# Kernel optimization log

Hardware: AMD Instinct MI355X
Metric: run time of the kernel (lower is better)

Reference implementation:

```python
import jax, jax.numpy as jnp
import numpy as np

B, T, D, L, H = 4096, 200, 128, 64, 128  # n_traj, time steps, input_dim, latent_dim, n_units


def _lin(key, fan_in, fan_out):
    s = 1.0 / np.sqrt(fan_in)
    kw, kb = jax.random.split(key)
    w = jax.random.uniform(kw, (fan_in, fan_out), jnp.float32, -s, s)
    b = jax.random.uniform(kb, (fan_out,), jnp.float32, -s, s)
    return w, b


def setup_inputs() -> dict:
    key = jax.random.key(0)
    ks = jax.random.split(key, 8)
    data = jax.random.normal(ks[0], (B, T, D), jnp.float32)
    time_steps = jax.random.uniform(ks[1], (T,), jnp.float32)
    cin = 2 * L + D
    ug_w1, ug_b1 = _lin(ks[2], cin, H)
    ug_w2, ug_b2 = _lin(ks[3], H, L)
    rg_w1, rg_b1 = _lin(ks[4], cin, H)
    rg_w2, rg_b2 = _lin(ks[5], H, L)
    ns_w1, ns_b1 = _lin(ks[6], cin, H)
    ns_w2, ns_b2 = _lin(ks[7], H, 2 * L)
    return dict(data=data, time_steps=time_steps,
                ug_w1=ug_w1, ug_b1=ug_b1, ug_w2=ug_w2, ug_b2=ug_b2,
                rg_w1=rg_w1, rg_b1=rg_b1, rg_w2=rg_w2, rg_b2=rg_b2,
                ns_w1=ns_w1, ns_b1=ns_b1, ns_w2=ns_w2, ns_b2=ns_b2)


def reference(data, time_steps,
              ug_w1, ug_b1, ug_w2, ug_b2,
              rg_w1, rg_b1, rg_w2, rg_b2,
              ns_w1, ns_b1, ns_w2, ns_b2):
    # GRUUnit (latent-ODE style): gates are 2-layer MLPs (Tanh hidden) over
    # concat([y_mean, y_logvar, x]); update/reset end in Sigmoid, new_state
    # net emits 2L (mean, |std|).
    def step(carry, x):  # x: [B, D]
        y, s = carry  # each [B, L]
        h = jnp.concatenate([y, s, x], axis=-1)  # [B, 2L+D]
        u = jax.nn.sigmoid(jnp.tanh(h @ ug_w1 + ug_b1) @ ug_w2 + ug_b2)
        r = jax.nn.sigmoid(jnp.tanh(h @ rg_w1 + rg_b1) @ rg_w2 + rg_b2)
        hc = jnp.concatenate([y * r, s * r, x], axis=-1)
        ns = jnp.tanh(hc @ ns_w1 + ns_b1) @ ns_w2 + ns_b2  # [B, 2L]
        new_mean = ns[:, :L]
        new_std = jnp.abs(ns[:, L:])
        y2 = (1.0 - u) * new_mean + u * y
        s2 = (1.0 - u) * new_std + u * s
        return (y2, s2), None

    y0 = jnp.zeros((data.shape[0], L), data.dtype)
    s0 = jnp.zeros((data.shape[0], L), data.dtype)
    xs = jnp.transpose(data, (1, 0, 2))  # [T, B, D]; scan over time
    (yT, sT), _ = jax.lax.scan(step, (y0, s0), xs)
    return yT, sT
```

## Files before the change

### kernel.cpp

```cpp
#include <hip/hip_runtime.h>
#include <hip/hip_bf16.h>


#define NB 4096
#define NT 200
#define ND 128
#define HS 528
#define TS 272

typedef __bf16 bf16;
typedef __attribute__((ext_vector_type(8))) __bf16 bf16x8;
typedef __attribute__((ext_vector_type(4))) __bf16 bf16x4;
typedef __attribute__((ext_vector_type(4))) float f32x4;

#define BAR() asm volatile("s_waitcnt lgkmcnt(0)\n\ts_barrier" ::: "memory")

__device__ __forceinline__ f32x4 mfma16(bf16x8 a, bf16x8 b, f32x4 c){
    return __builtin_amdgcn_mfma_f32_16x16x32_bf16(a, b, c, 0, 0, 0);
}
__device__ __forceinline__ float fast_tanh(float x){
    float e = __expf(2.f * x);
    return 1.f - 2.f * __builtin_amdgcn_rcpf(e + 1.f);
}
__device__ __forceinline__ float fast_sigmoid(float x){
    return __builtin_amdgcn_rcpf(1.f + __expf(-x));
}
__device__ __forceinline__ bf16x4 tanh4(f32x4 a){
    bf16x4 o;
    o[0] = (bf16)fast_tanh(a[0]);
    o[1] = (bf16)fast_tanh(a[1]);
    o[2] = (bf16)fast_tanh(a[2]);
    o[3] = (bf16)fast_tanh(a[3]);
    return o;
}
__device__ __forceinline__ f32x4 bias4(const float* b, int f){
    f32x4 r; r[0]=b[f]; r[1]=b[f+1]; r[2]=b[f+2]; r[3]=b[f+3]; return r;
}

__global__ __launch_bounds__(512, 2)
void vae_rnn(const float* __restrict__ data,
             const float* __restrict__ ug_w1, const float* __restrict__ ug_b1,
             const float* __restrict__ ug_w2, const float* __restrict__ ug_b2,
             const float* __restrict__ rg_w1, const float* __restrict__ rg_b1,
             const float* __restrict__ rg_w2, const float* __restrict__ rg_b2,
             const float* __restrict__ ns_w1, const float* __restrict__ ns_b1,
             const float* __restrict__ ns_w2, const float* __restrict__ ns_b2,
             float* __restrict__ out)
{
    __shared__ __align__(16) char h_lds [16 * HS];
    __shared__ __align__(16) char t_lds [16 * HS];
    __shared__ __align__(16) char tn_lds[16 * TS];
    __shared__ float u_lds[16][68];

    const int tid  = threadIdx.x;
    const int w    = tid >> 6;
    const int lane = tid & 63;
    const int lq   = lane >> 4;
    const int lc   = lane & 15;
    const int row0 = blockIdx.x * 16;

    const bool UG = (w < 4);
    const int fA = w * 32;
    const int fB = (w & 3) * 16;
    const int fC = w * 16;
    const int fD = w * 16;

    const float* W1 = UG ? ug_w1 : rg_w1;
    const float* B1 = UG ? ug_b1 : rg_b1;
    const float* W2 = UG ? ug_w2 : rg_w2;
    const float* B2 = UG ? ug_b2 : rg_b2;

    bf16x8 wAy[8], wAx[8]; f32x4 bA[2];
    #pragma unroll
    for (int j = 0; j < 2; ++j){
        int n = (fA + j*16 + lc) & 127;
        bA[j] = bias4(B1, (fA + j*16 + lq*4) & 127);
        #pragma unroll
        for (int kt = 0; kt < 4; ++kt){
            bf16x8 fy, fx;
            #pragma unroll
            for (int e = 0; e < 8; ++e){
                fy[e] = (bf16)W1[(      kt*32 + lq*8 + e)*128 + n];
                fx[e] = (bf16)W1[(128 + kt*32 + lq*8 + e)*128 + n];
            }
            wAy[kt*2 + j] = fy; wAx[kt*2 + j] = fx;
        }
    }
    bf16x8 wB[4]; f32x4 bB = bias4(B2, fB + lq*4);
    {
        int n = fB + lc;
        #pragma unroll
        for (int kt = 0; kt < 4; ++kt){
            bf16x8 f;
            #pragma unroll
            for (int e = 0; e < 8; ++e) f[e] = (bf16)W2[(kt*32 + lq*8 + e)*64 + n];
            wB[kt] = f;
        }
    }
    bf16x8 wCh[4], wCx[4]; f32x4 bC = bias4(ns_b1, fC + lq*4);
    {
        int n = fC + lc;
        #pragma unroll
        for (int kt = 0; kt < 4; ++kt){
            bf16x8 fh, fx;
            #pragma unroll
            for (int e = 0; e < 8; ++e){
                fh[e] = (bf16)ns_w1[(      kt*32 + lq*8 + e)*128 + n];
                fx[e] = (bf16)ns_w1[(128 + kt*32 + lq*8 + e)*128 + n];
            }
            wCh[kt] = fh; wCx[kt] = fx;
        }
    }
    bf16x8 wD[4]; f32x4 bD = bias4(ns_b2, fD + lq*4);
    {
        int n = fD + lc;
        #pragma unroll
        for (int kt = 0; kt < 4; ++kt){
            bf16x8 f;
            #pragma unroll
            for (int e = 0; e < 8; ++e) f[e] = (bf16)ns_w2[(kt*32 + lq*8 + e)*128 + n];
            wD[kt] = f;
        }
    }

    const char* h_ys_rd = h_lds + lc*HS + lq*16;
    const char* h_x_rd  = h_lds + lc*HS + 256 + lq*16;
    char*       t_wr    = t_lds + lc*HS + 2*(fA + lq*4);
    const char* t_rd    = t_lds + lc*HS + lq*16 + (UG ? 0 : 256);
    char*       tn_wr   = tn_lds + lc*TS + 2*(fC + lq*4);
    const char* tn_rd   = tn_lds + lc*TS + lq*16;
    char*       h_st_wr = h_lds + lc*HS + 2*(fD + lq*4);
    char*       ys_rw   = h_lds + lc*HS + 2*(fB + lq*4);

    const int xr = tid >> 5;
    const int xc = (tid & 31) << 2;
    const float* xsrc = data + (size_t)(row0 + xr) * (size_t)(NT * ND) + xc;
    char* x_wr = h_lds + xr*HS + 256 + 2*xc;

    *(bf16x4*)(h_lds + xr*HS + (tid & 31)*8) = (bf16x4){};
    {
        float4 x0 = *(const float4*)xsrc;
        bf16x4 xb = { (bf16)x0.x, (bf16)x0.y, (bf16)x0.z, (bf16)x0.w };
        *(bf16x4*)x_wr = xb;
    }
    BAR();
    f32x4 Ax0, Ax1, Cx;
    {
        Ax0 = bA[0]; Ax1 = bA[1]; Cx = bC;
        #pragma unroll
        for (int kt = 0; kt < 4; ++kt){
            bf16x8 xv = *(const bf16x8*)(h_x_rd + kt*64);
            Ax0 = mfma16(wAx[kt*2+0], xv, Ax0);
            Ax1 = mfma16(wAx[kt*2+1], xv, Ax1);
            Cx  = mfma16(wCx[kt],     xv, Cx);
        }
    }
    float4 xn = *(const float4*)(xsrc + ND);
    f32x4 st = {0.f,0.f,0.f,0.f};
    f32x4 ug_reg = {0.f,0.f,0.f,0.f};
    bf16x8 xf0, xf1, xf2, xf3;
    BAR();

    #pragma unroll 1
    for (int t = 0; t < NT; ++t){
        {
            f32x4 a0 = Ax0, a1 = Ax1;
            #pragma unroll
            for (int kt = 0; kt < 4; ++kt){
                bf16x8 hv = *(const bf16x8*)(h_ys_rd + kt*64);
                a0 = mfma16(wAy[kt*2+0], hv, a0);
                a1 = mfma16(wAy[kt*2+1], hv, a1);
            }
            *(bf16x4*)(t_wr +  0) = tanh4(a0);
            *(bf16x4*)(t_wr + 32) = tanh4(a1);
            bf16x4 xb = { (bf16)xn.x, (bf16)xn.y, (bf16)xn.z, (bf16)xn.w };
            *(bf16x4*)x_wr = xb;
            int t2 = (t + 2 < NT) ? (t + 2) : (NT - 1);
            xn = *(const float4*)(xsrc + (size_t)t2 * ND);
        }
        BAR();

        {
            f32x4 b0 = bB, b1 = {0.f,0.f,0.f,0.f};
            #pragma unroll
            for (int kt = 0; kt < 4; ++kt){
                bf16x8 tv = *(const bf16x8*)(t_rd + kt*64);
                if (kt & 1) b1 = mfma16(wB[kt], tv, b1);
                else        b0 = mfma16(wB[kt], tv, b0);
            }
            xf0 = *(const bf16x8*)(h_x_rd +   0);
            xf1 = *(const bf16x8*)(h_x_rd +  64);
            xf2 = *(const bf16x8*)(h_x_rd + 128);
            xf3 = *(const bf16x8*)(h_x_rd + 192);
            f32x4 ax0 = bA[0], ax1 = bA[1];
            ax0 = mfma16(wAx[0], xf0, ax0);  ax1 = mfma16(wAx[1], xf0, ax1);
            ax0 = mfma16(wAx[2], xf1, ax0);  ax1 = mfma16(wAx[3], xf1, ax1);
            ax0 = mfma16(wAx[4], xf2, ax0);  ax1 = mfma16(wAx[5], xf2, ax1);
            ax0 = mfma16(wAx[6], xf3, ax0);  ax1 = mfma16(wAx[7], xf3, ax1);
            Ax0 = ax0; Ax1 = ax1;
            f32x4 bs = b0 + b1;
            float g0 = fast_sigmoid(bs[0]);
            float g1 = fast_sigmoid(bs[1]);
            float g2 = fast_sigmoid(bs[2]);
            float g3 = fast_sigmoid(bs[3]);
            if (UG){
                ug_reg[0] = g0; ug_reg[1] = g1; ug_reg[2] = g2; ug_reg[3] = g3;
                *(f32x4*)&u_lds[lc][fB + lq*4] = ug_reg;
            } else {
                bf16x4 yv = *(const bf16x4*)(ys_rw);
                bf16x4 sv = *(const bf16x4*)(ys_rw + 128);
                bf16x4 hy = { (bf16)((float)yv[0]*g0), (bf16)((float)yv[1]*g1),
                              (bf16)((float)yv[2]*g2), (bf16)((float)yv[3]*g3) };
                bf16x4 hs = { (bf16)((float)sv[0]*g0), (bf16)((float)sv[1]*g1),
                              (bf16)((float)sv[2]*g2), (bf16)((float)sv[3]*g3) };
                *(bf16x4*)(ys_rw)       = hy;
                *(bf16x4*)(ys_rw + 128) = hs;
            }
        }
        BAR();

        {
            f32x4 c0 = Cx, c1 = {0.f,0.f,0.f,0.f};
            #pragma unroll
            for (int kt = 0; kt < 4; ++kt){
                bf16x8 hv = *(const bf16x8*)(h_ys_rd + kt*64);
                if (kt & 1) c1 = mfma16(wCh[kt], hv, c1);
                else        c0 = mfma16(wCh[kt], hv, c0);
            }
            f32x4 cx = bC;
            cx = mfma16(wCx[0], xf0, cx);
            cx = mfma16(wCx[1], xf1, cx);
            cx = mfma16(wCx[2], xf2, cx);
            cx = mfma16(wCx[3], xf3, cx);
            Cx = cx;
            f32x4 cs = c0 + c1;
            *(bf16x4*)tn_wr = tanh4(cs);
        }
        BAR();

        {
            f32x4 d0 = bD, d1 = {0.f,0.f,0.f,0.f};
            #pragma unroll
            for (int kt = 0; kt < 4; ++kt){
                bf16x8 tv = *(const bf16x8*)(tn_rd + kt*64);
                if (kt & 1) d1 = mfma16(wD[kt], tv, d1);
                else        d0 = mfma16(wD[kt], tv, d0);
            }
            f32x4 ds = d0 + d1;
            f32x4 uu = UG ? ug_reg : *(const f32x4*)&u_lds[lc][fB + lq*4];
            #pragma unroll
            for (int i = 0; i < 4; ++i){
                float v = UG ? ds[i] : fabsf(ds[i]);
                st[i] = fmaf(uu[i], st[i] - v, v);
            }
            bf16x4 hn = { (bf16)st[0], (bf16)st[1], (bf16)st[2], (bf16)st[3] };
            *(bf16x4*)h_st_wr = hn;
        }
        BAR();
    }

    {
        size_t gr = (size_t)(row0 + lc);
        float4 v = make_float4(st[0], st[1], st[2], st[3]);
        if (UG) *(float4*)&out[gr*64 + fD + lq*4] = v;
        else    *(float4*)&out[(size_t)NB*64 + gr*64 + (fD - 64) + lq*4] = v;
    }
}

extern "C" void kernel_launch(void* const* d_in, const int* in_sizes, int n_in,
                              void* d_out, int out_size, void* d_ws, size_t ws_size,
                              hipStream_t stream) {
    const float* data  = (const float*)d_in[0];
    const float* ug_w1 = (const float*)d_in[2];
    const float* ug_b1 = (const float*)d_in[3];
    const float* ug_w2 = (const float*)d_in[4];
    const float* ug_b2 = (const float*)d_in[5];
    const float* rg_w1 = (const float*)d_in[6];
    const float* rg_b1 = (const float*)d_in[7];
    const float* rg_w2 = (const float*)d_in[8];
    const float* rg_b2 = (const float*)d_in[9];
    const float* ns_w1 = (const float*)d_in[10];
    const float* ns_b1 = (const float*)d_in[11];
    const float* ns_w2 = (const float*)d_in[12];
    const float* ns_b2 = (const float*)d_in[13];

    hipLaunchKernelGGL(vae_rnn, dim3(NB/16), dim3(512), 0, stream,
                       data, ug_w1, ug_b1, ug_w2, ug_b2,
                       rg_w1, rg_b1, rg_w2, rg_b2,
                       ns_w1, ns_b1, ns_w2, ns_b2,
                       (float*)d_out);
}
```

Baseline: 324.0 us.

## Load x directly into MFMA fragment registers and rebalance x-projection across phases

Each lane now loads its own x slice from global memory straight into bf16x8 MFMA operand registers, so the x columns no longer pass through shared memory. The h and t shared tiles shrink or move accordingly, with strides swapped. The A-gate x projection moves to phase 3 and the C-net x projection moves to phase 4, and the global prefetch for t+2 is issued in phase 4. The goal is to remove the LDS traffic for x and even out the MFMA work between barriers, at the cost of more VGPRs (8 float4 per lane) and redundant global loads across waves.

```diff
diff --git a/kernel.cpp b/kernel.cpp
--- a/kernel.cpp
+++ b/kernel.cpp
@@ -5,8 +5,8 @@
 #define NB 4096
 #define NT 200
 #define ND 128
-#define HS 528
-#define TS 272
+#define HSB 272
+#define TSB 528
 
 typedef __bf16 bf16;
 typedef __attribute__((ext_vector_type(8))) __bf16 bf16x8;
@@ -47,9 +47,9 @@
              const float* __restrict__ ns_w2, const float* __restrict__ ns_b2,
              float* __restrict__ out)
 {
-    __shared__ __align__(16) char h_lds [16 * HS];
-    __shared__ __align__(16) char t_lds [16 * HS];
-    __shared__ __align__(16) char tn_lds[16 * TS];
+    __shared__ __align__(16) char h_lds [16 * HSB];
+    __shared__ __align__(16) char t_lds [16 * TSB];
+    __shared__ __align__(16) char tn_lds[16 * HSB];
     __shared__ float u_lds[16][68];
 
     const int tid  = threadIdx.x;
@@ -123,42 +123,48 @@
         }
     }
 
-    const char* h_ys_rd = h_lds + lc*HS + lq*16;
-    const char* h_x_rd  = h_lds + lc*HS + 256 + lq*16;
-    char*       t_wr    = t_lds + lc*HS + 2*(fA + lq*4);
-    const char* t_rd    = t_lds + lc*HS + lq*16 + (UG ? 0 : 256);
-    char*       tn_wr   = tn_lds + lc*TS + 2*(fC + lq*4);
-    const char* tn_rd   = tn_lds + lc*TS + lq*16;
-    char*       h_st_wr = h_lds + lc*HS + 2*(fD + lq*4);
-    char*       ys_rw   = h_lds + lc*HS + 2*(fB + lq*4);
-
-    const int xr = tid >> 5;
-    const int xc = (tid & 31) << 2;
-    const float* xsrc = data + (size_t)(row0 + xr) * (size_t)(NT * ND) + xc;
-    char* x_wr = h_lds + xr*HS + 256 + 2*xc;
-
-    *(bf16x4*)(h_lds + xr*HS + (tid & 31)*8) = (bf16x4){};
-    {
-        float4 x0 = *(const float4*)xsrc;
-        bf16x4 xb = { (bf16)x0.x, (bf16)x0.y, (bf16)x0.z, (bf16)x0.w };
-        *(bf16x4*)x_wr = xb;
-    }
-    BAR();
+    const char* h_ys_rd = h_lds + lc*HSB + lq*16;
+    char*       t_wr    = t_lds + lc*TSB + 2*(fA + lq*4);
+    const char* t_rd    = t_lds + lc*TSB + lq*16 + (UG ? 0 : 256);
+    char*       tn_wr   = tn_lds + lc*HSB + 2*(fC + lq*4);
+    const char* tn_rd   = tn_lds + lc*HSB + lq*16;
+    char*       h_st_wr = h_lds + lc*HSB + 2*(fD + lq*4);
+    char*       ys_rw   = h_lds + lc*HSB + 2*(fB + lq*4);
+
+    const float* xf_src = data + (size_t)(row0 + lc) * (size_t)(NT * ND) + lq*8;
+
+    *(bf16x4*)(h_lds + (tid >> 5)*HSB + (tid & 31)*8) = (bf16x4){};
+
+    float4 xg[8];
+    bf16x8 xb[4];
     f32x4 Ax0, Ax1, Cx;
     {
+        #pragma unroll
+        for (int kt = 0; kt < 4; ++kt){
+            xg[2*kt]   = *(const float4*)(xf_src + kt*32);
+            xg[2*kt+1] = *(const float4*)(xf_src + kt*32 + 4);
+        }
+        #pragma unroll
+        for (int kt = 0; kt < 4; ++kt){
+            float4 a = xg[2*kt], b = xg[2*kt+1];
+            xb[kt] = (bf16x8){ (bf16)a.x,(bf16)a.y,(bf16)a.z,(bf16)a.w,
+                               (bf16)b.x,(bf16)b.y,(bf16)b.z,(bf16)b.w };
+        }
         Ax0 = bA[0]; Ax1 = bA[1]; Cx = bC;
         #pragma unroll
         for (int kt = 0; kt < 4; ++kt){
-            bf16x8 xv = *(const bf16x8*)(h_x_rd + kt*64);
-            Ax0 = mfma16(wAx[kt*2+0], xv, Ax0);
-            Ax1 = mfma16(wAx[kt*2+1], xv, Ax1);
-            Cx  = mfma16(wCx[kt],     xv, Cx);
-        }
-    }
-    float4 xn = *(const float4*)(xsrc + ND);
+            Ax0 = mfma16(wAx[kt*2+0], xb[kt], Ax0);
+            Ax1 = mfma16(wAx[kt*2+1], xb[kt], Ax1);
+            Cx  = mfma16(wCx[kt],     xb[kt], Cx);
+        }
+        #pragma unroll
+        for (int kt = 0; kt < 4; ++kt){
+            xg[2*kt]   = *(const float4*)(xf_src + ND + kt*32);
+            xg[2*kt+1] = *(const float4*)(xf_src + ND + kt*32 + 4);
+        }
+    }
     f32x4 st = {0.f,0.f,0.f,0.f};
     f32x4 ug_reg = {0.f,0.f,0.f,0.f};
-    bf16x8 xf0, xf1, xf2, xf3;
     BAR();
 
     #pragma unroll 1
@@ -173,10 +179,6 @@
             }
             *(bf16x4*)(t_wr +  0) = tanh4(a0);
             *(bf16x4*)(t_wr + 32) = tanh4(a1);
-            bf16x4 xb = { (bf16)xn.x, (bf16)xn.y, (bf16)xn.z, (bf16)xn.w };
-            *(bf16x4*)x_wr = xb;
-            int t2 = (t + 2 < NT) ? (t + 2) : (NT - 1);
-            xn = *(const float4*)(xsrc + (size_t)t2 * ND);
         }
         BAR();
 
@@ -188,16 +190,12 @@
                 if (kt & 1) b1 = mfma16(wB[kt], tv, b1);
                 else        b0 = mfma16(wB[kt], tv, b0);
             }
-            xf0 = *(const bf16x8*)(h_x_rd +   0);
-            xf1 = *(const bf16x8*)(h_x_rd +  64);
-            xf2 = *(const bf16x8*)(h_x_rd + 128);
-            xf3 = *(const bf16x8*)(h_x_rd + 192);
-            f32x4 ax0 = bA[0], ax1 = bA[1];
-            ax0 = mfma16(wAx[0], xf0, ax0);  ax1 = mfma16(wAx[1], xf0, ax1);
-            ax0 = mfma16(wAx[2], xf1, ax0);  ax1 = mfma16(wAx[3], xf1, ax1);
-            ax0 = mfma16(wAx[4], xf2, ax0);  ax1 = mfma16(wAx[5], xf2, ax1);
-            ax0 = mfma16(wAx[6], xf3, ax0);  ax1 = mfma16(wAx[7], xf3, ax1);
-            Ax0 = ax0; Ax1 = ax1;
+            #pragma unroll
+            for (int kt = 0; kt < 4; ++kt){
+                float4 a = xg[2*kt], b = xg[2*kt+1];
+                xb[kt] = (bf16x8){ (bf16)a.x,(bf16)a.y,(bf16)a.z,(bf16)a.w,
+                                   (bf16)b.x,(bf16)b.y,(bf16)b.z,(bf16)b.w };
+            }
             f32x4 bs = b0 + b1;
             float g0 = fast_sigmoid(bs[0]);
             float g1 = fast_sigmoid(bs[1]);
@@ -227,18 +225,27 @@
                 if (kt & 1) c1 = mfma16(wCh[kt], hv, c1);
                 else        c0 = mfma16(wCh[kt], hv, c0);
             }
-            f32x4 cx = bC;
-            cx = mfma16(wCx[0], xf0, cx);
-            cx = mfma16(wCx[1], xf1, cx);
-            cx = mfma16(wCx[2], xf2, cx);
-            cx = mfma16(wCx[3], xf3, cx);
-            Cx = cx;
+            f32x4 ax0 = bA[0], ax1 = bA[1];
+            ax0 = mfma16(wAx[0], xb[0], ax0);  ax1 = mfma16(wAx[1], xb[0], ax1);
+            ax0 = mfma16(wAx[2], xb[1], ax0);  ax1 = mfma16(wAx[3], xb[1], ax1);
+            ax0 = mfma16(wAx[4], xb[2], ax0);  ax1 = mfma16(wAx[5], xb[2], ax1);
+            ax0 = mfma16(wAx[6], xb[3], ax0);  ax1 = mfma16(wAx[7], xb[3], ax1);
+            Ax0 = ax0; Ax1 = ax1;
             f32x4 cs = c0 + c1;
             *(bf16x4*)tn_wr = tanh4(cs);
         }
         BAR();
 
         {
+            int t2 = (t + 2 < NT) ? (t + 2) : (NT - 1);
+            const float* xp = xf_src + (size_t)t2 * ND;
+            #pragma unroll
+            for (int kt = 0; kt < 4; ++kt){
+                xg[2*kt]   = *(const float4*)(xp + kt*32);
+                xg[2*kt+1] = *(const float4*)(xp + kt*32 + 4);
+            }
+            f32x4 uu = ug_reg;
+            if (!UG) uu = *(const f32x4*)&u_lds[lc][fB + lq*4];
             f32x4 d0 = bD, d1 = {0.f,0.f,0.f,0.f};
             #pragma unroll
             for (int kt = 0; kt < 4; ++kt){
@@ -246,8 +253,13 @@
                 if (kt & 1) d1 = mfma16(wD[kt], tv, d1);
                 else        d0 = mfma16(wD[kt], tv, d0);
             }
+            f32x4 cx = bC;
+            cx = mfma16(wCx[0], xb[0], cx);
+            cx = mfma16(wCx[1], xb[1], cx);
+            cx = mfma16(wCx[2], xb[2], cx);
+            cx = mfma16(wCx[3], xb[3], cx);
+            Cx = cx;
             f32x4 ds = d0 + d1;
-            f32x4 uu = UG ? ug_reg : *(const f32x4*)&u_lds[lc][fB + lq*4];
             #pragma unroll
             for (int i = 0; i < 4; ++i){
                 float v = UG ? ds[i] : fabsf(ds[i]);
```

Result: slower. 517.1 us (+59.6%).
